# Optimization experiments

Measured on AMD Instinct MI355X. Metric: run time of the kernel, lower is better.

Reference implementation:

```python
import jax, jax.numpy as jnp
import numpy as np
from jax import lax

B, S, H = 4, 512, 2048
E, D = 16, 128
GH = E * D  # GRU hidden size = num_experts * router_dim
BAL_STRENGTH = 0.01


def _l2norm(v, eps):
    n = jnp.linalg.norm(v, axis=-1, keepdims=True)
    return v / jnp.maximum(n, eps)


def setup_inputs() -> dict:
    key = jax.random.key(0)
    ks = jax.random.split(key, 6)
    x = jax.random.normal(ks[0], (B, S, H), dtype=jnp.float32)
    hn = jax.random.normal(ks[1], (1, B, GH), dtype=jnp.float32)
    w_ih = jax.random.normal(ks[2], (3 * GH, H), dtype=jnp.float32) * 0.02
    w_hh = jax.random.normal(ks[3], (3 * GH, GH), dtype=jnp.float32) * 0.02
    w_expr = jax.random.normal(ks[4], (H, GH), dtype=jnp.float32) * 0.02
    expert_load_ema = jax.random.uniform(ks[5], (E,), dtype=jnp.float32)
    return {"x": x, "hn": hn, "w_ih": w_ih, "w_hh": w_hh,
            "w_expr": w_expr, "expert_load_ema": expert_load_ema, "top_k": 2}


def _gru(x, h0, w_ih, w_hh):
    # PyTorch GRU (no bias): gates ordered (r, z, n). Precompute input proj once.
    xi = jnp.einsum('bsh,gh->sbg', x, w_ih)  # [S,B,3*GH]
    xr, xz, xn = jnp.split(xi, 3, axis=-1)
    wr, wz, wn = jnp.split(w_hh, 3, axis=0)

    def step(h, xs):
        xr_t, xz_t, xn_t = xs
        r = jax.nn.sigmoid(xr_t + h @ wr.T)
        z = jax.nn.sigmoid(xz_t + h @ wz.T)
        n = jnp.tanh(xn_t + r * (h @ wn.T))
        h = (1.0 - z) * n + z * h
        return h, h

    hT, hs = lax.scan(step, h0, (xr, xz, xn))
    return hs.transpose(1, 0, 2), hT[None]  # [B,S,GH], [1,B,GH]


def reference(x, hn, w_ih, w_hh, w_expr, expert_load_ema, top_k):
    b, s, _ = x.shape
    e = expert_load_ema.shape[0]
    gh = w_hh.shape[1]
    d = gh // e

    routing_logits, hn_out = _gru(x, hn[0], w_ih, w_hh)

    expression_logits = (x @ w_expr).reshape(b, s, e, d)
    rout = routing_logits.reshape(b, s, e, d)
    rout = _l2norm(rout, 1e-12)  # F.normalize(dim=-1)

    # per-token expert gram matrix [B,S,E,E]
    gram = jnp.einsum('bsed,bsfd->bsef', rout, rout)
    diff = gram - jnp.eye(e, dtype=rout.dtype)
    diffn = _l2norm(diff, 1e-12)
    speciality_penalty = jnp.mean(jnp.sum(diffn ** 2, axis=(-2, -1)))

    # cosine sim (rout already unit-norm)
    en = jnp.maximum(jnp.linalg.norm(expression_logits, axis=-1), 1e-8)
    rn = jnp.maximum(jnp.linalg.norm(rout, axis=-1), 1e-8)
    cos = jnp.sum(expression_logits * rout, axis=-1) / (en * rn)
    cosine_similarities = 1.0 - cos  # [B,S,E]

    domain = (cosine_similarities * (1.0 + speciality_penalty)).reshape(b * s, e)
    top_vals, selected_experts = lax.top_k(domain, top_k)
    multiplier = jax.nn.softmax(top_vals.astype(jnp.float32), axis=-1).astype(domain.dtype)

    # ExpressionProjector orthogonal loss
    gw = w_expr.T @ w_expr
    expression_loss = jnp.mean((gw - jnp.eye(gh, dtype=w_expr.dtype)) ** 2)

    # training-mode EMA load-balance adjustment (no_grad in torch)
    ema = lax.stop_gradient(expert_load_ema)
    total = ema.sum()
    scores = jnp.where(total > 0, ema / jnp.maximum(total, 1e-12), jnp.zeros_like(ema))
    adjustment = scores * BAL_STRENGTH * e
    multiplier = multiplier - adjustment[selected_experts]

    return (multiplier, selected_experts, expression_logits, hn_out,
            speciality_penalty, cosine_similarities, expression_loss)
```

## Files before the change

kernel.cpp:

```cpp
#include <hip/hip_runtime.h>
#include <hip/hip_bf16.h>
#include <math.h>

#define BB 4
#define SS 512
#define HH 2048
#define EE 16
#define DD 128
#define GH 2048
#define G3 6144
#define NTOK 2048

#define LSTR 132
#define FPAD 32

__global__ __launch_bounds__(256) void gemm_abt(const float* __restrict__ A,
                                                const float* __restrict__ B,
                                                float* __restrict__ C,
                                                int M, int N, int K) {
  __shared__ float As[8][LSTR];
  __shared__ float Bs[8][LSTR];
  const int bm = blockIdx.y * 128, bn = blockIdx.x * 128;
  const int tid = threadIdx.x;
  const int lm = tid >> 1;
  const int kh = (tid & 1) * 4;
  const int tx = tid & 15, ty = tid >> 4;
  float acc[8][8] = {};
  const float* Arow = A + (size_t)(bm + lm) * K + kh;
  const float* Brow = B + (size_t)(bn + lm) * K + kh;
  for (int k0 = 0; k0 < K; k0 += 8) {
    float4 av = *(const float4*)(Arow + k0);
    float4 bv = *(const float4*)(Brow + k0);
    As[kh + 0][lm] = av.x; As[kh + 1][lm] = av.y; As[kh + 2][lm] = av.z; As[kh + 3][lm] = av.w;
    Bs[kh + 0][lm] = bv.x; Bs[kh + 1][lm] = bv.y; Bs[kh + 2][lm] = bv.z; Bs[kh + 3][lm] = bv.w;
    __syncthreads();
#pragma unroll
    for (int kk = 0; kk < 8; ++kk) {
      float a8[8], b8[8];
      *(float4*)(a8)     = *(const float4*)(&As[kk][ty * 8]);
      *(float4*)(a8 + 4) = *(const float4*)(&As[kk][ty * 8 + 4]);
      *(float4*)(b8)     = *(const float4*)(&Bs[kk][tx * 8]);
      *(float4*)(b8 + 4) = *(const float4*)(&Bs[kk][tx * 8 + 4]);
#pragma unroll
      for (int i = 0; i < 8; ++i)
#pragma unroll
        for (int j = 0; j < 8; ++j) acc[i][j] = fmaf(a8[i], b8[j], acc[i][j]);
    }
    __syncthreads();
  }
#pragma unroll
  for (int i = 0; i < 8; ++i) {
    float4 v0 = {acc[i][0], acc[i][1], acc[i][2], acc[i][3]};
    float4 v1 = {acc[i][4], acc[i][5], acc[i][6], acc[i][7]};
    float* crow = C + (size_t)(bm + ty * 8 + i) * N + bn + tx * 8;
    *(float4*)(crow)     = v0;
    *(float4*)(crow + 4) = v1;
  }
}

__global__ __launch_bounds__(256) void gemm_ab(const float* __restrict__ A,
                                               const float* __restrict__ B,
                                               float* __restrict__ C,
                                               int M, int N, int K) {
  __shared__ float As[8][LSTR];
  __shared__ float Bs[8][LSTR];
  const int bm = blockIdx.y * 128, bn = blockIdx.x * 128;
  const int tid = threadIdx.x;
  const int lm = tid >> 1;
  const int kh = (tid & 1) * 4;
  const int bk = tid >> 5;
  const int bn4 = (tid & 31) * 4;
  const int tx = tid & 15, ty = tid >> 4;
  float acc[8][8] = {};
  const float* Arow = A + (size_t)(bm + lm) * K + kh;
  for (int k0 = 0; k0 < K; k0 += 8) {
    float4 av = *(const float4*)(Arow + k0);
    float4 bv = *(const float4*)(B + (size_t)(k0 + bk) * N + bn + bn4);
    As[kh + 0][lm] = av.x; As[kh + 1][lm] = av.y; As[kh + 2][lm] = av.z; As[kh + 3][lm] = av.w;
    *(float4*)(&Bs[bk][bn4]) = bv;
    __syncthreads();
#pragma unroll
    for (int kk = 0; kk < 8; ++kk) {
      float a8[8], b8[8];
      *(float4*)(a8)     = *(const float4*)(&As[kk][ty * 8]);
      *(float4*)(a8 + 4) = *(const float4*)(&As[kk][ty * 8 + 4]);
      *(float4*)(b8)     = *(const float4*)(&Bs[kk][tx * 8]);
      *(float4*)(b8 + 4) = *(const float4*)(&Bs[kk][tx * 8 + 4]);
#pragma unroll
      for (int i = 0; i < 8; ++i)
#pragma unroll
        for (int j = 0; j < 8; ++j) acc[i][j] = fmaf(a8[i], b8[j], acc[i][j]);
    }
    __syncthreads();
  }
#pragma unroll
  for (int i = 0; i < 8; ++i) {
    float4 v0 = {acc[i][0], acc[i][1], acc[i][2], acc[i][3]};
    float4 v1 = {acc[i][4], acc[i][5], acc[i][6], acc[i][7]};
    float* crow = C + (size_t)(bm + ty * 8 + i) * N + bn + tx * 8;
    *(float4*)(crow)     = v0;
    *(float4*)(crow + 4) = v1;
  }
}

__global__ __launch_bounds__(256) void ata_loss(const float* __restrict__ A,
                                                float* __restrict__ el_accum,
                                                int N, int K) {
  __shared__ float As[8][LSTR];
  __shared__ float Bs[8][LSTR];
  __shared__ float red[256];
  const int bi = blockIdx.y * 128, bj = blockIdx.x * 128;
  const int tid = threadIdx.x;
  const int bk = tid >> 5;
  const int bn4 = (tid & 31) * 4;
  const int tx = tid & 15, ty = tid >> 4;
  float acc[8][8] = {};
  for (int k0 = 0; k0 < K; k0 += 8) {
    float4 av = *(const float4*)(A + (size_t)(k0 + bk) * N + bi + bn4);
    float4 bv = *(const float4*)(A + (size_t)(k0 + bk) * N + bj + bn4);
    *(float4*)(&As[bk][bn4]) = av;
    *(float4*)(&Bs[bk][bn4]) = bv;
    __syncthreads();
#pragma unroll
    for (int kk = 0; kk < 8; ++kk) {
      float a8[8], b8[8];
      *(float4*)(a8)     = *(const float4*)(&As[kk][ty * 8]);
      *(float4*)(a8 + 4) = *(const float4*)(&As[kk][ty * 8 + 4]);
      *(float4*)(b8)     = *(const float4*)(&Bs[kk][tx * 8]);
      *(float4*)(b8 + 4) = *(const float4*)(&Bs[kk][tx * 8 + 4]);
#pragma unroll
      for (int i = 0; i < 8; ++i)
#pragma unroll
        for (int j = 0; j < 8; ++j) acc[i][j] = fmaf(a8[i], b8[j], acc[i][j]);
    }
    __syncthreads();
  }
  float local = 0.f;
#pragma unroll
  for (int i = 0; i < 8; ++i) {
#pragma unroll
    for (int j = 0; j < 8; ++j) {
      int gi = bi + ty * 8 + i, gj = bj + tx * 8 + j;
      float d = acc[i][j] - ((gi == gj) ? 1.0f : 0.0f);
      local += d * d;
    }
  }
  red[tid] = local;
  __syncthreads();
  for (int s = 128; s > 0; s >>= 1) {
    if (tid < s) red[tid] += red[tid + s];
    __syncthreads();
  }
  if (tid == 0) atomicAdd(el_accum, red[0]);
}

__device__ inline float wred64(float v) {
#pragma unroll
  for (int o = 32; o; o >>= 1) v += __shfl_xor(v, o);
  return v;
}

__global__ __launch_bounds__(512, 2) void gru_persistent(
    const float* __restrict__ xi,
    const float* __restrict__ w_hh,
    const float* __restrict__ hn,
    float* __restrict__ hs,
    int* __restrict__ flags) {
  __shared__ __align__(16) float hsm[BB * GH];
  const int tid = threadIdx.x;
  const int wave = tid >> 6, lane = tid & 63;
  const int j = blockIdx.x * 8 + wave;

  float wgr[32], wgz[32], wgn[32];
  {
    const float* pr = w_hh + (size_t)j * GH;
    const float* pz = w_hh + (size_t)(GH + j) * GH;
    const float* pn = w_hh + (size_t)(2 * GH + j) * GH;
#pragma unroll
    for (int c = 0; c < 32; ++c) {
      int k = c * 64 + lane;
      wgr[c] = pr[k]; wgz[c] = pz[k]; wgn[c] = pn[k];
    }
  }
#pragma unroll
  for (int i = 0; i < 4; ++i) {
    int k = tid + i * 512;
    float4 v;
    v.x = hn[0 * GH + k]; v.y = hn[1 * GH + k];
    v.z = hn[2 * GH + k]; v.w = hn[3 * GH + k];
    *(float4*)(&hsm[k * 4]) = v;
  }
  __syncthreads();

  for (int s = 0; s < SS; ++s) {
    float xr = 0.f, xz = 0.f, xn_ = 0.f;
    if (lane < BB) {
      const float* xrow = xi + ((size_t)(lane * SS + s)) * G3;
      xr  = xrow[j];
      xz  = xrow[GH + j];
      xn_ = xrow[2 * GH + j];
    }

    float ar[BB] = {}, az[BB] = {}, an[BB] = {};
#pragma unroll
    for (int c = 0; c < 32; ++c) {
      float4 h4 = *(const float4*)(&hsm[(c * 64 + lane) * 4]);
      float w_r = wgr[c], w_z = wgz[c], w_n = wgn[c];
      ar[0] = fmaf(w_r, h4.x, ar[0]); az[0] = fmaf(w_z, h4.x, az[0]); an[0] = fmaf(w_n, h4.x, an[0]);
      ar[1] = fmaf(w_r, h4.y, ar[1]); az[1] = fmaf(w_z, h4.y, az[1]); an[1] = fmaf(w_n, h4.y, an[1]);
      ar[2] = fmaf(w_r, h4.z, ar[2]); az[2] = fmaf(w_z, h4.z, az[2]); an[2] = fmaf(w_n, h4.z, an[2]);
      ar[3] = fmaf(w_r, h4.w, ar[3]); az[3] = fmaf(w_z, h4.w, az[3]); an[3] = fmaf(w_n, h4.w, an[3]);
    }
#pragma unroll
    for (int b = 0; b < BB; ++b) { ar[b] = wred64(ar[b]); az[b] = wred64(az[b]); an[b] = wred64(an[b]); }

    if (lane < BB) {
      const int b = lane;
      float r = 1.0f / (1.0f + expf(-(xr + ar[b])));
      float z = 1.0f / (1.0f + expf(-(xz + az[b])));
      float n = tanhf(xn_ + r * an[b]);
      float hp = hsm[j * 4 + b];
      float hv = (1.0f - z) * n + z * hp;
      __hip_atomic_store(hs + ((size_t)(b * SS + s)) * GH + j, hv,
                         __ATOMIC_RELAXED, __HIP_MEMORY_SCOPE_AGENT);
    }

    if (s + 1 < SS) {
      __syncthreads();
      if (tid == 0)
        __hip_atomic_store(&flags[blockIdx.x * FPAD], s + 1,
                           __ATOMIC_RELAXED, __HIP_MEMORY_SCOPE_AGENT);
      if (wave == 0) {
        const int target = s + 1;
        for (;;) {
          int m0 = __hip_atomic_load(&flags[(lane      ) * FPAD], __ATOMIC_RELAXED, __HIP_MEMORY_SCOPE_AGENT);
          int m1 = __hip_atomic_load(&flags[(lane +  64) * FPAD], __ATOMIC_RELAXED, __HIP_MEMORY_SCOPE_AGENT);
          int m2 = __hip_atomic_load(&flags[(lane + 128) * FPAD], __ATOMIC_RELAXED, __HIP_MEMORY_SCOPE_AGENT);
          int m3 = __hip_atomic_load(&flags[(lane + 192) * FPAD], __ATOMIC_RELAXED, __HIP_MEMORY_SCOPE_AGENT);
          int mn = min(min(m0, m1), min(m2, m3));
#pragma unroll
          for (int o = 32; o; o >>= 1) mn = min(mn, __shfl_xor(mn, o));
          if (mn >= target) break;
        }
      }
      __syncthreads();
#pragma unroll
      for (int i = 0; i < 4; ++i) {
        int k = tid + i * 512;
        float4 v;
        v.x = hs[((size_t)(0 * SS + s)) * GH + k];
        v.y = hs[((size_t)(1 * SS + s)) * GH + k];
        v.z = hs[((size_t)(2 * SS + s)) * GH + k];
        v.w = hs[((size_t)(3 * SS + s)) * GH + k];
        *(float4*)(&hsm[k * 4]) = v;
      }
      __syncthreads();
    }
  }
}

__device__ inline float red16(float v) {
#pragma unroll
  for (int o = 8; o; o >>= 1) v += __shfl_xor(v, o);
  return v;
}

__global__ __launch_bounds__(256) void token_kernel(const float* __restrict__ hs,
                                                    const float* __restrict__ expr,
                                                    float* __restrict__ cos_out,
                                                    float* __restrict__ sp_accum) {
  __shared__ float routn[EE * 132];
  __shared__ float rowc[EE];
  const int t = blockIdx.x;
  const int tid = threadIdx.x;
  const int e = tid >> 4, sub = tid & 15;

  const float* rrow = hs + (size_t)t * GH + e * DD + sub * 8;
  float rv[8];
#pragma unroll
  for (int i = 0; i < 8; ++i) rv[i] = rrow[i];
  float ss = 0.f;
#pragma unroll
  for (int i = 0; i < 8; ++i) ss += rv[i] * rv[i];
  ss = red16(ss);
  float inv = 1.0f / fmaxf(sqrtf(ss), 1e-12f);
#pragma unroll
  for (int i = 0; i < 8; ++i) {
    rv[i] *= inv;
    routn[e * 132 + sub * 8 + i] = rv[i];
  }

  const float* erow = expr + (size_t)t * GH + e * DD + sub * 8;
  float en2 = 0.f, dot = 0.f;
#pragma unroll
  for (int i = 0; i < 8; ++i) {
    float ev = erow[i];
    en2 += ev * ev;
    dot += ev * rv[i];
  }
  en2 = red16(en2);
  dot = red16(dot);
  if (sub == 0) {
    float cosv = dot / fmaxf(sqrtf(en2), 1e-8f);
    cos_out[t * EE + e] = 1.0f - cosv;
  }
  __syncthreads();

  const int f = sub;
  float g = 0.f;
#pragma unroll
  for (int d = 0; d < DD; ++d)
    g = fmaf(routn[e * 132 + d], routn[f * 132 + d], g);
  float diff = g - ((e == f) ? 1.0f : 0.0f);
  float rowsum = red16(diff * diff);
  if (f == 0) {
    float nrm = fmaxf(sqrtf(rowsum), 1e-12f);
    rowc[e] = rowsum / (nrm * nrm);
  }
  __syncthreads();
  if (tid == 0) {
    float tok = 0.f;
#pragma unroll
    for (int i = 0; i < EE; ++i) tok += rowc[i];
    atomicAdd(sp_accum, tok);
  }
}

__global__ __launch_bounds__(256) void final_kernel(const float* __restrict__ hs,
                                                    const float* __restrict__ cos_out,
                                                    const float* __restrict__ ema,
                                                    const float* __restrict__ accum,
                                                    float* __restrict__ out_mult,
                                                    float* __restrict__ out_sel,
                                                    float* __restrict__ out_hn,
                                                    float* __restrict__ out_sp,
                                                    float* __restrict__ out_el) {
  const int gtid = blockIdx.x * 256 + threadIdx.x;
  if (gtid < BB * GH) {
    int b = gtid / GH, jj = gtid % GH;
    out_hn[gtid] = hs[((size_t)(b * SS + SS - 1)) * GH + jj];
  }
  if (gtid < NTOK) {
    float sp = accum[0] / (float)NTOK;
    float scale = 1.0f + sp;
    float dv[EE];
#pragma unroll
    for (int e = 0; e < EE; ++e) dv[e] = cos_out[gtid * EE + e] * scale;
    int i0 = 0; float v0 = dv[0];
#pragma unroll
    for (int e = 1; e < EE; ++e) { if (dv[e] > v0) { v0 = dv[e]; i0 = e; } }
    int i1 = -1; float v1 = -1e30f;
#pragma unroll
    for (int e = 0; e < EE; ++e) { if (e != i0 && dv[e] > v1) { v1 = dv[e]; i1 = e; } }
    float ex = expf(v1 - v0);
    float den = 1.0f + ex;
    float m0 = 1.0f / den, m1 = ex / den;
    float total = 0.f;
#pragma unroll
    for (int e = 0; e < EE; ++e) total += ema[e];
    float a0 = 0.f, a1 = 0.f;
    if (total > 0.f) {
      float invt = 1.0f / fmaxf(total, 1e-12f);
      a0 = ema[i0] * invt * 0.01f * (float)EE;
      a1 = ema[i1] * invt * 0.01f * (float)EE;
    }
    out_mult[gtid * 2 + 0] = m0 - a0;
    out_mult[gtid * 2 + 1] = m1 - a1;
    out_sel[gtid * 2 + 0] = (float)i0;
    out_sel[gtid * 2 + 1] = (float)i1;
  }
  if (gtid == 0) {
    out_sp[0] = accum[0] / (float)NTOK;
    out_el[0] = accum[1] / (float)(GH * GH);
  }
}

extern "C" void kernel_launch(void* const* d_in, const int* in_sizes, int n_in,
                              void* d_out, int out_size, void* d_ws, size_t ws_size,
                              hipStream_t stream) {
  const float* x      = (const float*)d_in[0];
  const float* hn     = (const float*)d_in[1];
  const float* w_ih   = (const float*)d_in[2];
  const float* w_hh   = (const float*)d_in[3];
  const float* w_expr = (const float*)d_in[4];
  const float* ema    = (const float*)d_in[5];
  float* out = (float*)d_out;

  float* out_mult = out;
  float* out_sel  = out + 4096;
  float* out_expr = out + 8192;
  float* out_hn   = out + 4202496;
  float* out_sp   = out + 4210688;
  float* out_cos  = out + 4210689;
  float* out_el   = out + 4243457;

  float* ws = (float*)d_ws;
  float* xi    = ws;
  float* hs    = ws + 12582912;
  float* accum = ws + 16777216;
  int*   flags = (int*)(ws + 16777220);

  hipMemsetAsync(accum, 0, (4 + 256 * FPAD) * sizeof(float), stream);

  gemm_abt<<<dim3(G3 / 128, NTOK / 128), 256, 0, stream>>>(x, w_ih, xi, NTOK, G3, HH);

  gemm_ab<<<dim3(GH / 128, NTOK / 128), 256, 0, stream>>>(x, w_expr, out_expr, NTOK, GH, HH);

  {
    void* args[] = {(void*)&xi, (void*)&w_hh, (void*)&hn, (void*)&hs, (void*)&flags};
    hipLaunchCooperativeKernel((void*)gru_persistent, dim3(256), dim3(512),
                               args, 0, stream);
  }

  ata_loss<<<dim3(GH / 128, GH / 128), 256, 0, stream>>>(w_expr, accum + 1, GH, HH);

  token_kernel<<<NTOK, 256, 0, stream>>>(hs, out_expr, out_cos, accum);

  final_kernel<<<(BB * GH + 255) / 256, 256, 0, stream>>>(hs, out_cos, ema, accum,
                                                          out_mult, out_sel, out_hn,
                                                          out_sp, out_el);
}
```

Measured before the change: 4.669 ms.

## Use split-bf16 MFMA for expression GEMM and loss; repack GRU hidden state exchange

Adds kernels that split x and transposed w_expr into bf16 hi/lo pairs and compute the expression GEMM and the w_expr^T w_expr orthogonality loss with three-pass bf16 MFMA instructions instead of FP32 SIMD loops. The bf16 path runs only when the workspace is large enough; otherwise it falls back to the old kernels. Separately, the persistent GRU now writes each step's hidden state in a block-packed layout. Each thread polls only its producer block's flag with s_sleep, rather than one wave polling all flags behind a block barrier, so the state is gathered in contiguous vector loads. This trades extra conversion passes, workspace and some bf16x3 precision loss for matrix-core throughput and cheaper inter-step synchronisation.

```diff
diff --git a/kernel.cpp b/kernel.cpp
--- a/kernel.cpp
+++ b/kernel.cpp
@@ -13,6 +13,10 @@
 
 #define LSTR 132
 #define FPAD 32
+#define KS 40
+
+typedef __attribute__((ext_vector_type(8))) short short8;
+typedef __attribute__((ext_vector_type(4))) float f32x4;
 
 __global__ __launch_bounds__(256) void gemm_abt(const float* __restrict__ A,
                                                 const float* __restrict__ B,
@@ -154,6 +158,198 @@
   if (tid == 0) atomicAdd(el_accum, red[0]);
 }
 
+__device__ inline void bf16_split(float v, unsigned short& hi, unsigned short& lo) {
+  unsigned u = __float_as_uint(v);
+  unsigned r = u + 0x7FFFu + ((u >> 16) & 1u);
+  hi = (unsigned short)(r >> 16);
+  float rem = v - __uint_as_float((unsigned)hi << 16);
+  lo = (unsigned short)(__float_as_uint(rem) >> 16);
+}
+
+__global__ __launch_bounds__(256) void split_mat(const float* __restrict__ A,
+                                                 unsigned short* __restrict__ Hh,
+                                                 unsigned short* __restrict__ Hl,
+                                                 int n) {
+  int i = blockIdx.x * 256 + threadIdx.x;
+  int stride = gridDim.x * 256;
+  for (; i < n; i += stride) {
+    unsigned short hi, lo;
+    bf16_split(A[i], hi, lo);
+    Hh[i] = hi; Hl[i] = lo;
+  }
+}
+
+__global__ __launch_bounds__(256) void transpose_split(const float* __restrict__ A,
+                                                       unsigned short* __restrict__ Th,
+                                                       unsigned short* __restrict__ Tl) {
+  __shared__ float tile[64][65];
+  const int bx = blockIdx.x * 64, by = blockIdx.y * 64;
+  const int tx = threadIdx.x & 63, ty = threadIdx.x >> 6;
+#pragma unroll
+  for (int i = 0; i < 16; ++i) {
+    int r = ty + i * 4;
+    tile[r][tx] = A[(size_t)(by + r) * GH + bx + tx];
+  }
+  __syncthreads();
+#pragma unroll
+  for (int i = 0; i < 16; ++i) {
+    int r = ty + i * 4;
+    unsigned short hi, lo;
+    bf16_split(tile[tx][r], hi, lo);
+    Th[(size_t)(bx + r) * HH + by + tx] = hi;
+    Tl[(size_t)(bx + r) * HH + by + tx] = lo;
+  }
+}
+
+__global__ __launch_bounds__(256) void gemm_abt_bf16(
+    const unsigned short* __restrict__ Ah, const unsigned short* __restrict__ Al,
+    const unsigned short* __restrict__ Bh, const unsigned short* __restrict__ Bl,
+    float* __restrict__ C, int M, int N, int K) {
+  __shared__ unsigned short Ahs[128 * KS], Als[128 * KS];
+  __shared__ unsigned short Bhs[128 * KS], Bls[128 * KS];
+  const int tid = threadIdx.x;
+  const int wv = tid >> 6, lane = tid & 63;
+  const int qr = wv >> 1, qc = wv & 1;
+  const int m16 = lane & 15, q = lane >> 4;
+  const int bm = blockIdx.y * 128, bn = blockIdx.x * 128;
+  const int sr = tid >> 1, sh = (tid & 1) * 16;
+  f32x4 zero = {0.f, 0.f, 0.f, 0.f};
+  f32x4 acc[4][4];
+#pragma unroll
+  for (int i = 0; i < 4; ++i)
+#pragma unroll
+    for (int j = 0; j < 4; ++j) acc[i][j] = zero;
+
+  for (int k0 = 0; k0 < K; k0 += 32) {
+    const size_t ga = (size_t)(bm + sr) * K + k0 + sh;
+    const size_t gb = (size_t)(bn + sr) * K + k0 + sh;
+    short8 a0 = *(const short8*)(Ah + ga);
+    short8 a1 = *(const short8*)(Ah + ga + 8);
+    short8 l0 = *(const short8*)(Al + ga);
+    short8 l1 = *(const short8*)(Al + ga + 8);
+    short8 b0 = *(const short8*)(Bh + gb);
+    short8 b1 = *(const short8*)(Bh + gb + 8);
+    short8 m0 = *(const short8*)(Bl + gb);
+    short8 m1 = *(const short8*)(Bl + gb + 8);
+    __syncthreads();
+    *(short8*)&Ahs[sr * KS + sh]     = a0;
+    *(short8*)&Ahs[sr * KS + sh + 8] = a1;
+    *(short8*)&Als[sr * KS + sh]     = l0;
+    *(short8*)&Als[sr * KS + sh + 8] = l1;
+    *(short8*)&Bhs[sr * KS + sh]     = b0;
+    *(short8*)&Bhs[sr * KS + sh + 8] = b1;
+    *(short8*)&Bls[sr * KS + sh]     = m0;
+    *(short8*)&Bls[sr * KS + sh + 8] = m1;
+    __syncthreads();
+    short8 afh[4], afl[4], bfh[4], bfl[4];
+#pragma unroll
+    for (int t = 0; t < 4; ++t) {
+      const int raddr = (qr * 64 + t * 16 + m16) * KS + q * 8;
+      const int caddr = (qc * 64 + t * 16 + m16) * KS + q * 8;
+      afh[t] = *(const short8*)&Ahs[raddr];
+      afl[t] = *(const short8*)&Als[raddr];
+      bfh[t] = *(const short8*)&Bhs[caddr];
+      bfl[t] = *(const short8*)&Bls[caddr];
+    }
+#pragma unroll
+    for (int tm = 0; tm < 4; ++tm)
+#pragma unroll
+      for (int tn = 0; tn < 4; ++tn) {
+        acc[tm][tn] = __builtin_amdgcn_mfma_f32_16x16x32_bf16(afh[tm], bfh[tn], acc[tm][tn], 0, 0, 0);
+        acc[tm][tn] = __builtin_amdgcn_mfma_f32_16x16x32_bf16(afh[tm], bfl[tn], acc[tm][tn], 0, 0, 0);
+        acc[tm][tn] = __builtin_amdgcn_mfma_f32_16x16x32_bf16(afl[tm], bfh[tn], acc[tm][tn], 0, 0, 0);
+      }
+  }
+#pragma unroll
+  for (int tm = 0; tm < 4; ++tm)
+#pragma unroll
+    for (int tn = 0; tn < 4; ++tn)
+#pragma unroll
+      for (int r = 0; r < 4; ++r)
+        C[(size_t)(bm + qr * 64 + tm * 16 + q * 4 + r) * N +
+          bn + qc * 64 + tn * 16 + m16] = acc[tm][tn][r];
+}
+
+__global__ __launch_bounds__(256) void ata_bf16(
+    const unsigned short* __restrict__ Th, const unsigned short* __restrict__ Tl,
+    float* __restrict__ el_accum, int N, int K) {
+  __shared__ unsigned short Ahs[128 * KS], Als[128 * KS];
+  __shared__ unsigned short Bhs[128 * KS], Bls[128 * KS];
+  __shared__ float red[256];
+  const int tid = threadIdx.x;
+  const int wv = tid >> 6, lane = tid & 63;
+  const int qr = wv >> 1, qc = wv & 1;
+  const int m16 = lane & 15, q = lane >> 4;
+  const int bi = blockIdx.y * 128, bj = blockIdx.x * 128;
+  const int sr = tid >> 1, sh = (tid & 1) * 16;
+  f32x4 zero = {0.f, 0.f, 0.f, 0.f};
+  f32x4 acc[4][4];
+#pragma unroll
+  for (int i = 0; i < 4; ++i)
+#pragma unroll
+    for (int j = 0; j < 4; ++j) acc[i][j] = zero;
+
+  for (int k0 = 0; k0 < K; k0 += 32) {
+    const size_t ga = (size_t)(bi + sr) * K + k0 + sh;
+    const size_t gb = (size_t)(bj + sr) * K + k0 + sh;
+    short8 a0 = *(const short8*)(Th + ga);
+    short8 a1 = *(const short8*)(Th + ga + 8);
+    short8 l0 = *(const short8*)(Tl + ga);
+    short8 l1 = *(const short8*)(Tl + ga + 8);
+    short8 b0 = *(const short8*)(Th + gb);
+    short8 b1 = *(const short8*)(Th + gb + 8);
+    short8 m0 = *(const short8*)(Tl + gb);
+    short8 m1 = *(const short8*)(Tl + gb + 8);
+    __syncthreads();
+    *(short8*)&Ahs[sr * KS + sh]     = a0;
+    *(short8*)&Ahs[sr * KS + sh + 8] = a1;
+    *(short8*)&Als[sr * KS + sh]     = l0;
+    *(short8*)&Als[sr * KS + sh + 8] = l1;
+    *(short8*)&Bhs[sr * KS + sh]     = b0;
+    *(short8*)&Bhs[sr * KS + sh + 8] = b1;
+    *(short8*)&Bls[sr * KS + sh]     = m0;
+    *(short8*)&Bls[sr * KS + sh + 8] = m1;
+    __syncthreads();
+    short8 afh[4], afl[4], bfh[4], bfl[4];
+#pragma unroll
+    for (int t = 0; t < 4; ++t) {
+      const int raddr = (qr * 64 + t * 16 + m16) * KS + q * 8;
+      const int caddr = (qc * 64 + t * 16 + m16) * KS + q * 8;
+      afh[t] = *(const short8*)&Ahs[raddr];
+      afl[t] = *(const short8*)&Als[raddr];
+      bfh[t] = *(const short8*)&Bhs[caddr];
+      bfl[t] = *(const short8*)&Bls[caddr];
+    }
+#pragma unroll
+    for (int tm = 0; tm < 4; ++tm)
+#pragma unroll
+      for (int tn = 0; tn < 4; ++tn) {
+        acc[tm][tn] = __builtin_amdgcn_mfma_f32_16x16x32_bf16(afh[tm], bfh[tn], acc[tm][tn], 0, 0, 0);
+        acc[tm][tn] = __builtin_amdgcn_mfma_f32_16x16x32_bf16(afh[tm], bfl[tn], acc[tm][tn], 0, 0, 0);
+        acc[tm][tn] = __builtin_amdgcn_mfma_f32_16x16x32_bf16(afl[tm], bfh[tn], acc[tm][tn], 0, 0, 0);
+      }
+  }
+  float local = 0.f;
+#pragma unroll
+  for (int tm = 0; tm < 4; ++tm)
+#pragma unroll
+    for (int tn = 0; tn < 4; ++tn)
+#pragma unroll
+      for (int r = 0; r < 4; ++r) {
+        int gi = bi + qr * 64 + tm * 16 + q * 4 + r;
+        int gj = bj + qc * 64 + tn * 16 + m16;
+        float d = acc[tm][tn][r] - ((gi == gj) ? 1.0f : 0.0f);
+        local += d * d;
+      }
+  red[tid] = local;
+  __syncthreads();
+  for (int s = 128; s > 0; s >>= 1) {
+    if (tid < s) red[tid] += red[tid + s];
+    __syncthreads();
+  }
+  if (tid == 0) atomicAdd(el_accum, red[0]);
+}
+
 __device__ inline float wred64(float v) {
 #pragma unroll
   for (int o = 32; o; o >>= 1) v += __shfl_xor(v, o);
@@ -164,7 +360,7 @@
     const float* __restrict__ xi,
     const float* __restrict__ w_hh,
     const float* __restrict__ hn,
-    float* __restrict__ hs,
+    float* __restrict__ hsx,
     int* __restrict__ flags) {
   __shared__ __align__(16) float hsm[BB * GH];
   const int tid = threadIdx.x;
@@ -221,8 +417,8 @@
       float n = tanhf(xn_ + r * an[b]);
       float hp = hsm[j * 4 + b];
       float hv = (1.0f - z) * n + z * hp;
-      __hip_atomic_store(hs + ((size_t)(b * SS + s)) * GH + j, hv,
-                         __ATOMIC_RELAXED, __HIP_MEMORY_SCOPE_AGENT);
+      __hip_atomic_store(hsx + (((size_t)s * 256 + blockIdx.x) * BB + b) * 8 + (j & 7),
+                         hv, __ATOMIC_RELAXED, __HIP_MEMORY_SCOPE_AGENT);
     }
 
     if (s + 1 < SS) {
@@ -230,30 +426,22 @@
       if (tid == 0)
         __hip_atomic_store(&flags[blockIdx.x * FPAD], s + 1,
                            __ATOMIC_RELAXED, __HIP_MEMORY_SCOPE_AGENT);
-      if (wave == 0) {
-        const int target = s + 1;
-        for (;;) {
-          int m0 = __hip_atomic_load(&flags[(lane      ) * FPAD], __ATOMIC_RELAXED, __HIP_MEMORY_SCOPE_AGENT);
-          int m1 = __hip_atomic_load(&flags[(lane +  64) * FPAD], __ATOMIC_RELAXED, __HIP_MEMORY_SCOPE_AGENT);
-          int m2 = __hip_atomic_load(&flags[(lane + 128) * FPAD], __ATOMIC_RELAXED, __HIP_MEMORY_SCOPE_AGENT);
-          int m3 = __hip_atomic_load(&flags[(lane + 192) * FPAD], __ATOMIC_RELAXED, __HIP_MEMORY_SCOPE_AGENT);
-          int mn = min(min(m0, m1), min(m2, m3));
-#pragma unroll
-          for (int o = 32; o; o >>= 1) mn = min(mn, __shfl_xor(mn, o));
-          if (mn >= target) break;
-        }
-      }
-      __syncthreads();
-#pragma unroll
-      for (int i = 0; i < 4; ++i) {
-        int k = tid + i * 512;
-        float4 v;
-        v.x = hs[((size_t)(0 * SS + s)) * GH + k];
-        v.y = hs[((size_t)(1 * SS + s)) * GH + k];
-        v.z = hs[((size_t)(2 * SS + s)) * GH + k];
-        v.w = hs[((size_t)(3 * SS + s)) * GH + k];
-        *(float4*)(&hsm[k * 4]) = v;
-      }
+      const int p = tid >> 1;
+      const int c4 = (tid & 1) * 4;
+      const int want = s + 1;
+      while (__hip_atomic_load(&flags[p * FPAD], __ATOMIC_RELAXED,
+                               __HIP_MEMORY_SCOPE_AGENT) < want)
+        __builtin_amdgcn_s_sleep(1);
+      const float* line = hsx + ((size_t)s * 256 + p) * 32 + c4;
+      float4 v0 = *(const float4*)(line + 0 * 8);
+      float4 v1 = *(const float4*)(line + 1 * 8);
+      float4 v2 = *(const float4*)(line + 2 * 8);
+      float4 v3 = *(const float4*)(line + 3 * 8);
+      const int k0 = tid * 4;
+      *(float4*)(&hsm[(k0 + 0) * 4]) = float4{v0.x, v1.x, v2.x, v3.x};
+      *(float4*)(&hsm[(k0 + 1) * 4]) = float4{v0.y, v1.y, v2.y, v3.y};
+      *(float4*)(&hsm[(k0 + 2) * 4]) = float4{v0.z, v1.z, v2.z, v3.z};
+      *(float4*)(&hsm[(k0 + 3) * 4]) = float4{v0.w, v1.w, v2.w, v3.w};
       __syncthreads();
     }
   }
@@ -265,20 +453,21 @@
   return v;
 }
 
-__global__ __launch_bounds__(256) void token_kernel(const float* __restrict__ hs,
+__global__ __launch_bounds__(256) void token_kernel(const float* __restrict__ hsx,
                                                     const float* __restrict__ expr,
                                                     float* __restrict__ cos_out,
                                                     float* __restrict__ sp_accum) {
   __shared__ float routn[EE * 132];
   __shared__ float rowc[EE];
   const int t = blockIdx.x;
+  const int b = t / SS, s = t % SS;
   const int tid = threadIdx.x;
   const int e = tid >> 4, sub = tid & 15;
 
-  const float* rrow = hs + (size_t)t * GH + e * DD + sub * 8;
+  const float* rrow = hsx + ((size_t)s * 256 + e * 16 + sub) * 32 + b * 8;
   float rv[8];
-#pragma unroll
-  for (int i = 0; i < 8; ++i) rv[i] = rrow[i];
+  *(float4*)(rv)     = *(const float4*)(rrow);
+  *(float4*)(rv + 4) = *(const float4*)(rrow + 4);
   float ss = 0.f;
 #pragma unroll
   for (int i = 0; i < 8; ++i) ss += rv[i] * rv[i];
@@ -326,7 +515,7 @@
   }
 }
 
-__global__ __launch_bounds__(256) void final_kernel(const float* __restrict__ hs,
+__global__ __launch_bounds__(256) void final_kernel(const float* __restrict__ hsx,
                                                     const float* __restrict__ cos_out,
                                                     const float* __restrict__ ema,
                                                     const float* __restrict__ accum,
@@ -337,8 +526,8 @@
                                                     float* __restrict__ out_el) {
   const int gtid = blockIdx.x * 256 + threadIdx.x;
   if (gtid < BB * GH) {
-    int b = gtid / GH, jj = gtid % GH;
-    out_hn[gtid] = hs[((size_t)(b * SS + SS - 1)) * GH + jj];
+    int b = gtid / GH, k = gtid % GH;
+    out_hn[gtid] = hsx[((size_t)(SS - 1) * 256 + (k >> 3)) * 32 + b * 8 + (k & 7)];
   }
   if (gtid < NTOK) {
     float sp = accum[0] / (float)NTOK;
@@ -396,27 +585,40 @@
 
   float* ws = (float*)d_ws;
   float* xi    = ws;
-  float* hs    = ws + 12582912;
+  float* hsx   = ws + 12582912;
   float* accum = ws + 16777216;
   int*   flags = (int*)(ws + 16777220);
+  unsigned short* xh  = (unsigned short*)(ws + 16785920);
+  unsigned short* xl  = (unsigned short*)(ws + 18883072);
+  unsigned short* wth = (unsigned short*)(ws + 20980224);
+  unsigned short* wtl = (unsigned short*)(ws + 23077376);
+  const size_t need_bytes = (size_t)25174528 * 4;
+  const bool bf16path = ws_size >= need_bytes;
 
   hipMemsetAsync(accum, 0, (4 + 256 * FPAD) * sizeof(float), stream);
 
   gemm_abt<<<dim3(G3 / 128, NTOK / 128), 256, 0, stream>>>(x, w_ih, xi, NTOK, G3, HH);
 
-  gemm_ab<<<dim3(GH / 128, NTOK / 128), 256, 0, stream>>>(x, w_expr, out_expr, NTOK, GH, HH);
+  if (bf16path) {
+    split_mat<<<4096, 256, 0, stream>>>(x, xh, xl, NTOK * HH);
+    transpose_split<<<dim3(GH / 64, HH / 64), 256, 0, stream>>>(w_expr, wth, wtl);
+    gemm_abt_bf16<<<dim3(GH / 128, NTOK / 128), 256, 0, stream>>>(
+        xh, xl, wth, wtl, out_expr, NTOK, GH, HH);
+    ata_bf16<<<dim3(GH / 128, GH / 128), 256, 0, stream>>>(wth, wtl, accum + 1, GH, HH);
+  } else {
+    gemm_ab<<<dim3(GH / 128, NTOK / 128), 256, 0, stream>>>(x, w_expr, out_expr, NTOK, GH, HH);
+    ata_loss<<<dim3(GH / 128, GH / 128), 256, 0, stream>>>(w_expr, accum + 1, GH, HH);
+  }
 
   {
-    void* args[] = {(void*)&xi, (void*)&w_hh, (void*)&hn, (void*)&hs, (void*)&flags};
+    void* args[] = {(void*)&xi, (void*)&w_hh, (void*)&hn, (void*)&hsx, (void*)&flags};
     hipLaunchCooperativeKernel((void*)gru_persistent, dim3(256), dim3(512),
                                args, 0, stream);
   }
 
-  ata_loss<<<dim3(GH / 128, GH / 128), 256, 0, stream>>>(w_expr, accum + 1, GH, HH);
-
-  token_kernel<<<NTOK, 256, 0, stream>>>(hs, out_expr, out_cos, accum);
-
-  final_kernel<<<(BB * GH + 255) / 256, 256, 0, stream>>>(hs, out_cos, ema, accum,
+  token_kernel<<<NTOK, 256, 0, stream>>>(hsx, out_expr, out_cos, accum);
+
+  final_kernel<<<(BB * GH + 255) / 256, 256, 0, stream>>>(hsx, out_cos, ema, accum,
                                                           out_mult, out_sel, out_hn,
                                                           out_sp, out_el);
 }
```

Result: faster. 3.990 ms (-14.6%).
